# Kernel tuning notes

Hardware: AMD Instinct MI355X
Metric: run time of the kernel (lower is better)

The kernel has to match this reference:

```python
import jax, jax.numpy as jnp
import numpy as np

R_MAX, S_MAX, TOKEN_Z = 32, 2, 128
N_IN = 4 * (R_MAX + 1) + 2 * (S_MAX + 1) + 1  # 139
B, L = 1, 1024


def setup_inputs() -> dict:
    key = jax.random.key(0)
    k1, k2, k3, k4, k5 = jax.random.split(key, 5)
    asym_id = jnp.sort(jax.random.randint(k1, (B, L), 0, 8), axis=-1)
    residue_index = jnp.sort(jax.random.randint(k2, (B, L), 0, 512), axis=-1)
    entity_id = jax.random.randint(k3, (B, L), 0, 4)
    token_index = jnp.arange(B * L, dtype=jnp.int64 if jax.config.jax_enable_x64 else jnp.int32).reshape(B, L)
    sym_id = jax.random.randint(k4, (B, L), 0, 4)
    cyclic_period = jnp.zeros((B, L), dtype=jnp.int32)
    W = jax.random.normal(k5, (N_IN, TOKEN_Z), dtype=jnp.float32) * 0.02
    return {
        "asym_id": asym_id,
        "residue_index": residue_index,
        "entity_id": entity_id,
        "token_index": token_index,
        "sym_id": sym_id,
        "cyclic_period": cyclic_period,
        "W": W,
    }


def reference(asym_id, residue_index, entity_id, token_index, sym_id, cyclic_period, W):
    # Pairwise boolean masks [B, L, L]
    same_chain = asym_id[:, :, None] == asym_id[:, None, :]
    same_residue = residue_index[:, :, None] == residue_index[:, None, :]
    same_entity = entity_id[:, :, None] == entity_id[:, None, :]

    rel_pos = residue_index[:, :, None] - residue_index[:, None, :]
    # Cyclic wrap: period=10000 where cyclic_period<=0 is a no-op for |rel_pos|<5000
    period = jnp.where(cyclic_period > 0, cyclic_period, 10000)[:, None, :]
    rel_pos = rel_pos - (period * jnp.round(rel_pos / period)).astype(rel_pos.dtype)

    d_residue = jnp.clip(rel_pos + R_MAX, 0, 2 * R_MAX)
    d_residue = jnp.where(same_chain, d_residue, 2 * R_MAX + 1)

    d_token = jnp.clip(token_index[:, :, None] - token_index[:, None, :] + R_MAX, 0, 2 * R_MAX)
    d_token = jnp.where(same_chain & same_residue, d_token, 2 * R_MAX + 1)

    d_chain = jnp.clip(sym_id[:, :, None] - sym_id[:, None, :] + S_MAX, 0, 2 * S_MAX)
    d_chain = jnp.where(same_chain, 2 * S_MAX + 1, d_chain)

    # onehot(d) @ W == gather of W rows: fuse concat+onehot+linear into gathers + sum.
    n_rel = 2 * R_MAX + 2  # 66
    n_ch = 2 * S_MAX + 2   # 6
    W_pos = W[:n_rel]
    W_tok = W[n_rel:2 * n_rel]
    w_ent = W[2 * n_rel]
    W_ch = W[2 * n_rel + 1:2 * n_rel + 1 + n_ch]

    p = (W_pos[d_residue]
         + W_tok[d_token]
         + same_entity[..., None].astype(W.dtype) * w_ent
         + W_ch[d_chain])  # [B, L, L, token_z]
    return p
```

## Files before the change

kernel.cpp:

```cpp
#include <hip/hip_runtime.h>

#define TZ 128
#define JT 256
#define R_MAX 32
#define S_MAX 2

typedef float v4f __attribute__((ext_vector_type(4)));


__global__ __launch_bounds__(256) void relpos_kernel(
    const int* __restrict__ asym, const int* __restrict__ resi,
    const int* __restrict__ ent,  const int* __restrict__ tok,
    const int* __restrict__ sym,  const int* __restrict__ cyc,
    const float* __restrict__ W,  float* __restrict__ out, int L)
{
    __shared__ unsigned int sidx[JT];

    const int i   = blockIdx.x;
    const int j0  = blockIdx.y * JT;
    const int tid = threadIdx.x;

    {
        const int j  = j0 + tid;
        const int ai = asym[i], aj = asym[j];
        const int ri = resi[i], rj = resi[j];
        const int ei = ent[i],  ej = ent[j];
        const int ti = tok[i],  tj = tok[j];
        const int si = sym[i],  sj = sym[j];
        const int cj = cyc[j];

        const bool same_chain = (ai == aj);
        const bool same_res   = (ri == rj);
        const bool same_ent   = (ei == ej);

        int rel = ri - rj;
        const int period = (cj > 0) ? cj : 10000;
        const float q = rintf((float)rel / (float)period);
        rel -= (int)((float)period * q);

        int dr = rel + R_MAX;
        dr = dr < 0 ? 0 : (dr > 2 * R_MAX ? 2 * R_MAX : dr);
        if (!same_chain) dr = 2 * R_MAX + 1;

        int dt = ti - tj + R_MAX;
        dt = dt < 0 ? 0 : (dt > 2 * R_MAX ? 2 * R_MAX : dt);
        if (!(same_chain && same_res)) dt = 2 * R_MAX + 1;

        int dc = si - sj + S_MAX;
        dc = dc < 0 ? 0 : (dc > 2 * S_MAX ? 2 * S_MAX : dc);
        if (same_chain) dc = 2 * S_MAX + 1;

        sidx[tid] = (unsigned)dr | ((unsigned)dt << 8) | ((unsigned)dc << 16)
                  | ((unsigned)(same_ent ? 1u : 0u) << 24);
    }
    __syncthreads();

    const int zq = tid & 31;
    const int jr = tid >> 5;

    const v4f* __restrict__ Wv = (const v4f*)W;
    const v4f we = Wv[132 * 32 + zq];

    v4f* __restrict__ outv = (v4f*)(out + ((size_t)i * (size_t)L + (size_t)j0) * TZ);

    #pragma unroll 4
    for (int it = 0; it < JT / 8; ++it) {
        const int jl = it * 8 + jr;
        const unsigned pk = sidx[jl];
        const int dr = pk & 0xFF;
        const int dt = (pk >> 8) & 0xFF;
        const int dc = (pk >> 16) & 0xFF;
        const float se = (pk >> 24) ? 1.0f : 0.0f;

        const v4f a = Wv[dr * 32 + zq];
        const v4f b = Wv[(66 + dt) * 32 + zq];
        const v4f c = Wv[(133 + dc) * 32 + zq];

        const v4f r = a + b + c + se * we;

        __builtin_nontemporal_store(r, &outv[jl * 32 + zq]);
    }
}

extern "C" void kernel_launch(void* const* d_in, const int* in_sizes, int n_in,
                              void* d_out, int out_size, void* d_ws, size_t ws_size,
                              hipStream_t stream) {
    const int* asym = (const int*)d_in[0];
    const int* resi = (const int*)d_in[1];
    const int* ent  = (const int*)d_in[2];
    const int* tok  = (const int*)d_in[3];
    const int* sym  = (const int*)d_in[4];
    const int* cyc  = (const int*)d_in[5];
    const float* W  = (const float*)d_in[6];
    float* out      = (float*)d_out;

    const int L = in_sizes[0];
    dim3 grid(L, L / JT);
    dim3 block(256);
    relpos_kernel<<<grid, block, 0, stream>>>(asym, resi, ent, tok, sym, cyc, W, out, L);
}
```

Measured before the change: 539.7 us.

## Stage W in LDS and process four query rows per block

Copies the whole 139x128 weight table into shared memory once per block and has each block handle four i rows instead of one, so the table load and the j-side index reads are amortised over more output. Gathers now read W from LDS instead of global/L1, and the per-pair division is replaced by a precomputed reciprocal multiply. In exchange each block uses about 71 KB of LDS, which caps residency at two blocks per CU, and the grid shrinks fourfold. The kernel is dominated by its 512 MB output write, so the gain may be small.

```diff
diff --git a/kernel.cpp b/kernel.cpp
--- a/kernel.cpp
+++ b/kernel.cpp
@@ -2,83 +2,97 @@
 
 #define TZ 128
 #define JT 256
+#define IT 4
 #define R_MAX 32
 #define S_MAX 2
+#define NROW 139
 
 typedef float v4f __attribute__((ext_vector_type(4)));
 
-
-__global__ __launch_bounds__(256) void relpos_kernel(
+__global__ __launch_bounds__(256, 2) void relpos_kernel(
     const int* __restrict__ asym, const int* __restrict__ resi,
     const int* __restrict__ ent,  const int* __restrict__ tok,
     const int* __restrict__ sym,  const int* __restrict__ cyc,
     const float* __restrict__ W,  float* __restrict__ out, int L)
 {
-    __shared__ unsigned int sidx[JT];
+    __shared__ v4f sW[NROW * 32];
+    __shared__ unsigned int sidx[IT * JT];
 
-    const int i   = blockIdx.x;
+    const int i0  = blockIdx.x * IT;
     const int j0  = blockIdx.y * JT;
     const int tid = threadIdx.x;
 
+    const v4f* __restrict__ Wv = (const v4f*)W;
+
+    for (int idx = tid; idx < NROW * 32; idx += 256)
+        sW[idx] = Wv[idx];
+
     {
         const int j  = j0 + tid;
-        const int ai = asym[i], aj = asym[j];
-        const int ri = resi[i], rj = resi[j];
-        const int ei = ent[i],  ej = ent[j];
-        const int ti = tok[i],  tj = tok[j];
-        const int si = sym[i],  sj = sym[j];
-        const int cj = cyc[j];
+        const int aj = asym[j], rj = resi[j], ej = ent[j];
+        const int tj = tok[j],  sj = sym[j],  cj = cyc[j];
+        const int period = (cj > 0) ? cj : 10000;
+        const float inv_p = 1.0f / (float)period;
 
-        const bool same_chain = (ai == aj);
-        const bool same_res   = (ri == rj);
-        const bool same_ent   = (ei == ej);
+        #pragma unroll
+        for (int ii = 0; ii < IT; ++ii) {
+            const int i  = i0 + ii;
+            const int ai = asym[i], ri = resi[i], ei = ent[i];
+            const int ti = tok[i],  si = sym[i];
 
-        int rel = ri - rj;
-        const int period = (cj > 0) ? cj : 10000;
-        const float q = rintf((float)rel / (float)period);
-        rel -= (int)((float)period * q);
+            const bool same_chain = (ai == aj);
+            const bool same_res   = (ri == rj);
+            const bool same_ent   = (ei == ej);
 
-        int dr = rel + R_MAX;
-        dr = dr < 0 ? 0 : (dr > 2 * R_MAX ? 2 * R_MAX : dr);
-        if (!same_chain) dr = 2 * R_MAX + 1;
+            int rel = ri - rj;
+            const float q = rintf((float)rel * inv_p);
+            rel -= (int)((float)period * q);
 
-        int dt = ti - tj + R_MAX;
-        dt = dt < 0 ? 0 : (dt > 2 * R_MAX ? 2 * R_MAX : dt);
-        if (!(same_chain && same_res)) dt = 2 * R_MAX + 1;
+            int dr = rel + R_MAX;
+            dr = dr < 0 ? 0 : (dr > 2 * R_MAX ? 2 * R_MAX : dr);
+            if (!same_chain) dr = 2 * R_MAX + 1;
 
-        int dc = si - sj + S_MAX;
-        dc = dc < 0 ? 0 : (dc > 2 * S_MAX ? 2 * S_MAX : dc);
-        if (same_chain) dc = 2 * S_MAX + 1;
+            int dt = ti - tj + R_MAX;
+            dt = dt < 0 ? 0 : (dt > 2 * R_MAX ? 2 * R_MAX : dt);
+            if (!(same_chain && same_res)) dt = 2 * R_MAX + 1;
 
-        sidx[tid] = (unsigned)dr | ((unsigned)dt << 8) | ((unsigned)dc << 16)
-                  | ((unsigned)(same_ent ? 1u : 0u) << 24);
+            int dc = si - sj + S_MAX;
+            dc = dc < 0 ? 0 : (dc > 2 * S_MAX ? 2 * S_MAX : dc);
+            if (same_chain) dc = 2 * S_MAX + 1;
+
+            sidx[ii * JT + tid] = (unsigned)dr | ((unsigned)dt << 8)
+                                | ((unsigned)dc << 16)
+                                | ((unsigned)(same_ent ? 1u : 0u) << 24);
+        }
     }
-    __syncthreads();
 
     const int zq = tid & 31;
     const int jr = tid >> 5;
-
-    const v4f* __restrict__ Wv = (const v4f*)W;
     const v4f we = Wv[132 * 32 + zq];
 
-    v4f* __restrict__ outv = (v4f*)(out + ((size_t)i * (size_t)L + (size_t)j0) * TZ);
+    __syncthreads();
 
-    #pragma unroll 4
-    for (int it = 0; it < JT / 8; ++it) {
-        const int jl = it * 8 + jr;
-        const unsigned pk = sidx[jl];
-        const int dr = pk & 0xFF;
-        const int dt = (pk >> 8) & 0xFF;
-        const int dc = (pk >> 16) & 0xFF;
-        const float se = (pk >> 24) ? 1.0f : 0.0f;
+    for (int ii = 0; ii < IT; ++ii) {
+        v4f* __restrict__ outp =
+            (v4f*)(out + ((size_t)(i0 + ii) * (size_t)L + (size_t)j0) * TZ);
 
-        const v4f a = Wv[dr * 32 + zq];
-        const v4f b = Wv[(66 + dt) * 32 + zq];
-        const v4f c = Wv[(133 + dc) * 32 + zq];
+        #pragma unroll 4
+        for (int it = 0; it < JT / 8; ++it) {
+            const int jl = it * 8 + jr;
+            const unsigned pk = sidx[ii * JT + jl];
+            const int dr = pk & 0xFF;
+            const int dt = (pk >> 8) & 0xFF;
+            const int dc = (pk >> 16) & 0xFF;
+            const float se = (pk >> 24) ? 1.0f : 0.0f;
 
-        const v4f r = a + b + c + se * we;
+            const v4f a = sW[dr * 32 + zq];
+            const v4f b = sW[(66 + dt) * 32 + zq];
+            const v4f c = sW[(133 + dc) * 32 + zq];
 
-        __builtin_nontemporal_store(r, &outv[jl * 32 + zq]);
+            const v4f r = a + b + c + se * we;
+
+            __builtin_nontemporal_store(r, &outp[jl * 32 + zq]);
+        }
     }
 }
 
@@ -95,7 +109,7 @@
     float* out      = (float*)d_out;
 
     const int L = in_sizes[0];
-    dim3 grid(L, L / JT);
+    dim3 grid(L / IT, L / JT);
     dim3 block(256);
     relpos_kernel<<<grid, block, 0, stream>>>(asym, resi, ent, tok, sym, cyc, W, out, L);
 }
```

After: 541.6 us. No clear change (+0.4%).
